# Performance work log

Measured on AMD Instinct MI355X. Metric: run time of the kernel, lower is better.

## Reference

```python
import jax, jax.numpy as jnp
import numpy as np
from jax import lax

DT = 0.1  # forward() default dt


def setup_inputs() -> dict:
    key = jax.random.key(0)
    k1, k2, k3 = jax.random.split(key, 3)
    B, S = 256, 65536
    strain = jax.random.normal(k1, (B, S), dtype=jnp.float32)
    strain_rate = jax.random.normal(k2, (B, S), dtype=jnp.float32)
    log_E = jnp.zeros((1,), dtype=jnp.float32)            # E = 1.0
    log_eta = jnp.log(jnp.full((1,), 10.0, jnp.float32))  # eta = 10.0
    return {"strain": strain, "strain_rate": strain_rate,
            "log_E": log_E, "log_eta": log_eta}


def reference(strain, strain_rate, log_E, log_eta):
    # Maxwell element: stress[0] = E*strain[0] + eta*rate[0]
    #                  stress[t] = a*stress[t-1] + E*(strain[t]-strain[t-1]),  a = exp(-dt/tau)
    E = jnp.exp(log_E)          # (1,)
    eta = jnp.exp(log_eta)      # (1,)
    tau = eta / E
    a = jnp.exp(-DT / tau)      # (1,) constant decay

    B, S = strain.shape
    # driving term u[t]
    u0 = E * strain[:, :1] + eta * strain_rate[:, :1]          # (B,1)
    u_rest = E * (strain[:, 1:] - strain[:, :-1])              # (B,S-1)
    u = jnp.concatenate([u0, u_rest], axis=1)                  # (B,S)
    # decay coeffs: first step has no history
    A = jnp.concatenate([jnp.ones((B, 1), strain.dtype),
                         jnp.broadcast_to(a, (B, S - 1))], axis=1)

    def combine(x, y):
        a1, b1 = x
        a2, b2 = y
        return a1 * a2, b2 + a2 * b1

    _, stress = lax.associative_scan(combine, (A, u), axis=1)  # (B,S)
    return stress
```

## Files before the change

### kernel.cpp

```cpp
#include <hip/hip_runtime.h>
#include <math.h>


#define DT_F     0.1f
#define S_LEN    65536
#define B_ROWS   256
#define CHUNK    8192
#define WARM     2048
#define CPR      (S_LEN / CHUNK)

__global__ __launch_bounds__(256) void maxwell_scan(
    const float* __restrict__ strain,
    const float* __restrict__ rate,
    const float* __restrict__ log_E,
    const float* __restrict__ log_eta,
    float* __restrict__ out)
{
    const int lane = threadIdx.x & 63;
    const int wid  = blockIdx.x * 4 + (threadIdx.x >> 6);
    const int row  = wid / CPR;
    const int c    = wid % CPR;

    const float E   = __expf(log_E[0]);
    const float eta = __expf(log_eta[0]);
    const float lam = -DT_F * E / eta;
    const float a   = __expf(lam);
    const float a2 = a * a, a3 = a2 * a, a4 = a2 * a2;
    const float a8 = a4 * a4, a16 = a8 * a8, a32 = a16 * a16;
    const float a64 = a32 * a32, a128 = a64 * a64, a256 = a128 * a128;
    const float alane = __expf(lam * (float)(4 * lane));

    const int rowbase = row * S_LEN;
    const int t0   = c * CHUNK;
    const int tw   = (c == 0) ? 0 : (t0 - WARM);
    const int tend = t0 + CHUNK;

    const float4* s4 = (const float4*)(strain + rowbase);
    float4*       o4 = (float4*)(out + rowbase);

    float G = 0.0f;
    float last_strain = (tw > 0) ? strain[rowbase + tw - 1] : 0.0f;
    const float u_first = E * strain[rowbase] + eta * rate[rowbase];

    for (int t = tw; t < tend; t += 256) {
        float4 f = s4[(t >> 2) + lane];

        float pf   = __shfl_up(f.w, 1);
        float prev = (lane == 0) ? last_strain : pf;
        float u0 = E * (f.x - prev);
        if (t == 0 && lane == 0) u0 = u_first;
        float u1 = E * (f.y - f.x);
        float u2 = E * (f.z - f.y);
        float u3 = E * (f.w - f.z);

        float s0 = u0;
        float s1 = fmaf(a, s0, u1);
        float s2 = fmaf(a, s1, u2);
        float s3 = fmaf(a, s2, u3);

        float D = s3, v;
        v = __shfl_up(D, 1);  D += (lane >= 1)  ? a4   * v : 0.0f;
        v = __shfl_up(D, 2);  D += (lane >= 2)  ? a8   * v : 0.0f;
        v = __shfl_up(D, 4);  D += (lane >= 4)  ? a16  * v : 0.0f;
        v = __shfl_up(D, 8);  D += (lane >= 8)  ? a32  * v : 0.0f;
        v = __shfl_up(D, 16); D += (lane >= 16) ? a64  * v : 0.0f;
        v = __shfl_up(D, 32); D += (lane >= 32) ? a128 * v : 0.0f;

        float Dm1 = __shfl_up(D, 1);
        float C = (lane == 0) ? 0.0f : Dm1;
        C = fmaf(alane, G, C);

        float o0 = fmaf(a,  C, s0);
        float o1 = fmaf(a2, C, s1);
        float o2 = fmaf(a3, C, s2);
        float o3 = fmaf(a4, C, s3);

        if (t >= t0) {
            o4[(t >> 2) + lane] = make_float4(o0, o1, o2, o3);
        }

        G = fmaf(a256, G, __shfl(D, 63));
        last_strain = __shfl(f.w, 63);
    }
}

extern "C" void kernel_launch(void* const* d_in, const int* in_sizes, int n_in,
                              void* d_out, int out_size, void* d_ws, size_t ws_size,
                              hipStream_t stream) {
    const float* strain  = (const float*)d_in[0];
    const float* rate    = (const float*)d_in[1];
    const float* log_E   = (const float*)d_in[2];
    const float* log_eta = (const float*)d_in[3];
    float* out = (float*)d_out;

    const int total_chunks = B_ROWS * CPR;
    const int blocks = total_chunks / 4;
    maxwell_scan<<<blocks, 256, 0, stream>>>(strain, rate, log_E, log_eta, out);
}
```

Baseline: 176.8 us.

## Process eight elements per lane, shrink chunks, use nontemporal stores

Each lane now handles eight consecutive elements (two float4 loads) per iteration instead of four, so each wave iteration covers 512 elements and the wave-level shuffle scan is amortised over twice the work. The chunk size drops from 8192 to 2048 with a 1024-element warm-up, which raises the number of waves and the parallelism available across the GPU. Output is written with nontemporal stores to avoid polluting the cache. The trade-off is more redundant warm-up reads relative to useful output (half a chunk instead of a quarter), and a shorter warm-up that relies on the decay factor making truncation error negligible.

```diff
diff --git a/kernel.cpp b/kernel.cpp
--- a/kernel.cpp
+++ b/kernel.cpp
@@ -5,9 +5,11 @@
 #define DT_F     0.1f
 #define S_LEN    65536
 #define B_ROWS   256
-#define CHUNK    8192
-#define WARM     2048
+#define CHUNK    2048
+#define WARM     1024
 #define CPR      (S_LEN / CHUNK)
+
+typedef float nfloat4 __attribute__((ext_vector_type(4)));
 
 __global__ __launch_bounds__(256) void maxwell_scan(
     const float* __restrict__ strain,
@@ -25,62 +27,73 @@
     const float eta = __expf(log_eta[0]);
     const float lam = -DT_F * E / eta;
     const float a   = __expf(lam);
-    const float a2 = a * a, a3 = a2 * a, a4 = a2 * a2;
-    const float a8 = a4 * a4, a16 = a8 * a8, a32 = a16 * a16;
-    const float a64 = a32 * a32, a128 = a64 * a64, a256 = a128 * a128;
-    const float alane = __expf(lam * (float)(4 * lane));
+    const float a2 = a * a,     a3 = a2 * a,    a4 = a2 * a2;
+    const float a5 = a4 * a,    a6 = a4 * a2,   a7 = a4 * a3,   a8 = a4 * a4;
+    const float a16 = a8 * a8,  a32 = a16 * a16, a64 = a32 * a32;
+    const float a128 = a64 * a64, a256 = a128 * a128, a512 = a256 * a256;
+    const float alane = __expf(lam * (float)(8 * lane));
 
     const int rowbase = row * S_LEN;
     const int t0   = c * CHUNK;
     const int tw   = (c == 0) ? 0 : (t0 - WARM);
     const int tend = t0 + CHUNK;
 
-    const float4* s4 = (const float4*)(strain + rowbase);
-    float4*       o4 = (float4*)(out + rowbase);
+    const nfloat4* s4 = (const nfloat4*)(strain + rowbase);
+    nfloat4*       o4 = (nfloat4*)(out + rowbase);
 
     float G = 0.0f;
     float last_strain = (tw > 0) ? strain[rowbase + tw - 1] : 0.0f;
     const float u_first = E * strain[rowbase] + eta * rate[rowbase];
 
-    for (int t = tw; t < tend; t += 256) {
-        float4 f = s4[(t >> 2) + lane];
+    for (int t = tw; t < tend; t += 512) {
+        const int vi = (t >> 2) + 2 * lane;
+        nfloat4 f0 = s4[vi];
+        nfloat4 f1 = s4[vi + 1];
 
-        float pf   = __shfl_up(f.w, 1);
+        float pf   = __shfl_up(f1.w, 1);
         float prev = (lane == 0) ? last_strain : pf;
-        float u0 = E * (f.x - prev);
+        float u0 = E * (f0.x - prev);
         if (t == 0 && lane == 0) u0 = u_first;
-        float u1 = E * (f.y - f.x);
-        float u2 = E * (f.z - f.y);
-        float u3 = E * (f.w - f.z);
+        float u1 = E * (f0.y - f0.x);
+        float u2 = E * (f0.z - f0.y);
+        float u3 = E * (f0.w - f0.z);
+        float u4 = E * (f1.x - f0.w);
+        float u5 = E * (f1.y - f1.x);
+        float u6 = E * (f1.z - f1.y);
+        float u7 = E * (f1.w - f1.z);
 
         float s0 = u0;
         float s1 = fmaf(a, s0, u1);
         float s2 = fmaf(a, s1, u2);
         float s3 = fmaf(a, s2, u3);
+        float s4v = fmaf(a, s3, u4);
+        float s5 = fmaf(a, s4v, u5);
+        float s6 = fmaf(a, s5, u6);
+        float s7 = fmaf(a, s6, u7);
 
-        float D = s3, v;
-        v = __shfl_up(D, 1);  D += (lane >= 1)  ? a4   * v : 0.0f;
-        v = __shfl_up(D, 2);  D += (lane >= 2)  ? a8   * v : 0.0f;
-        v = __shfl_up(D, 4);  D += (lane >= 4)  ? a16  * v : 0.0f;
-        v = __shfl_up(D, 8);  D += (lane >= 8)  ? a32  * v : 0.0f;
-        v = __shfl_up(D, 16); D += (lane >= 16) ? a64  * v : 0.0f;
-        v = __shfl_up(D, 32); D += (lane >= 32) ? a128 * v : 0.0f;
+        float D = s7, v;
+        v = __shfl_up(D, 1);  D += (lane >= 1)  ? a8   * v : 0.0f;
+        v = __shfl_up(D, 2);  D += (lane >= 2)  ? a16  * v : 0.0f;
+        v = __shfl_up(D, 4);  D += (lane >= 4)  ? a32  * v : 0.0f;
+        v = __shfl_up(D, 8);  D += (lane >= 8)  ? a64  * v : 0.0f;
+        v = __shfl_up(D, 16); D += (lane >= 16) ? a128 * v : 0.0f;
+        v = __shfl_up(D, 32); D += (lane >= 32) ? a256 * v : 0.0f;
 
         float Dm1 = __shfl_up(D, 1);
         float C = (lane == 0) ? 0.0f : Dm1;
         C = fmaf(alane, G, C);
 
-        float o0 = fmaf(a,  C, s0);
-        float o1 = fmaf(a2, C, s1);
-        float o2 = fmaf(a3, C, s2);
-        float o3 = fmaf(a4, C, s3);
-
         if (t >= t0) {
-            o4[(t >> 2) + lane] = make_float4(o0, o1, o2, o3);
+            nfloat4 o0 = { fmaf(a,  C, s0),  fmaf(a2, C, s1),
+                           fmaf(a3, C, s2),  fmaf(a4, C, s3) };
+            nfloat4 o1 = { fmaf(a5, C, s4v), fmaf(a6, C, s5),
+                           fmaf(a7, C, s6),  fmaf(a8, C, s7) };
+            __builtin_nontemporal_store(o0, &o4[vi]);
+            __builtin_nontemporal_store(o1, &o4[vi + 1]);
         }
 
-        G = fmaf(a256, G, __shfl(D, 63));
-        last_strain = __shfl(f.w, 63);
+        G = fmaf(a512, G, __shfl(D, 63));
+        last_strain = __shfl(f1.w, 63);
     }
 }
 
```

Result: faster. 164.5 us (-6.9%).

## Reformulate Maxwell scan on raw strain with DPP row scans and smaller chunks

Applied to the files above, without the earlier changes.

Rewrites the recurrence algebraically to scan the strain values directly (stress = E*strain + E(a-1)*scan of previous strain, plus a decaying rate term), which removes the neighbour-difference shuffle. The intra-wave scan uses DPP row shifts within 16-lane rows plus readlane to combine rows, replacing six cross-lane shuffles with conditional masks. Chunks shrink to 2048 with a 1024-element warm-up and all payload loads are issued up front, fully unrolled, for more parallelism and memory-level overlap. This trades a higher warm-up overhead ratio and different floating-point rounding for cheaper per-step lane communication.

```diff
diff --git a/kernel.cpp b/kernel.cpp
--- a/kernel.cpp
+++ b/kernel.cpp
@@ -2,12 +2,23 @@
 #include <math.h>
 
 
-#define DT_F     0.1f
-#define S_LEN    65536
-#define B_ROWS   256
-#define CHUNK    8192
-#define WARM     2048
-#define CPR      (S_LEN / CHUNK)
+#define DT_F  0.1f
+#define S_LEN 65536
+#define B_ROWS 256
+#define CHUNK 2048
+#define WARM  1024
+#define CPR   (S_LEN / CHUNK)
+
+typedef float nfloat4 __attribute__((ext_vector_type(4)));
+
+template<int N>
+__device__ __forceinline__ float dpp_shr(float x) {
+    return __int_as_float(__builtin_amdgcn_update_dpp(
+        0, __float_as_int(x), 0x110 + N, 0xF, 0xF, false));
+}
+__device__ __forceinline__ float rdl(float x, int l) {
+    return __int_as_float(__builtin_amdgcn_readlane(__float_as_int(x), l));
+}
 
 __global__ __launch_bounds__(256) void maxwell_scan(
     const float* __restrict__ strain,
@@ -25,63 +36,90 @@
     const float eta = __expf(log_eta[0]);
     const float lam = -DT_F * E / eta;
     const float a   = __expf(lam);
-    const float a2 = a * a, a3 = a2 * a, a4 = a2 * a2;
-    const float a8 = a4 * a4, a16 = a8 * a8, a32 = a16 * a16;
-    const float a64 = a32 * a32, a128 = a64 * a64, a256 = a128 * a128;
+    const float a2 = a * a, a3 = a2 * a, a4 = a2 * a2, a8 = a4 * a4;
+    const float a16 = a8 * a8, a32 = a16 * a16, a64 = a32 * a32;
+    const float a128 = a64 * a64, a256 = a128 * a128;
+    const float cc = E * (a - 1.0f);
+    const float cca1 = cc * a, cca2 = cc * a2, cca3 = cc * a3;
+
+    const int  lrow = lane & 15;
     const float alane = __expf(lam * (float)(4 * lane));
+    const float wX    = __expf(lam * (float)(4 * lrow));
+    const bool row0 = (lrow == 0);
+    const bool ge16 = lane >= 16, ge32 = lane >= 32, ge48 = lane >= 48;
 
     const int rowbase = row * S_LEN;
-    const int t0   = c * CHUNK;
-    const int tw   = (c == 0) ? 0 : (t0 - WARM);
-    const int tend = t0 + CHUNK;
+    const int t0 = c * CHUNK;
+    const nfloat4* s4 = (const nfloat4*)(strain + rowbase);
+    nfloat4*       o4 = (nfloat4*)(out + rowbase);
 
-    const float4* s4 = (const float4*)(strain + rowbase);
-    float4*       o4 = (float4*)(out + rowbase);
+    const int vp = (t0 >> 2) + lane;
+    nfloat4 p0 = s4[vp +   0], p1 = s4[vp +  64], p2 = s4[vp + 128], p3 = s4[vp + 192];
+    nfloat4 p4 = s4[vp + 256], p5 = s4[vp + 320], p6 = s4[vp + 384], p7 = s4[vp + 448];
 
-    float G = 0.0f;
-    float last_strain = (tw > 0) ? strain[rowbase + tw - 1] : 0.0f;
-    const float u_first = E * strain[rowbase] + eta * rate[rowbase];
+    float S = 0.0f;
 
-    for (int t = tw; t < tend; t += 256) {
-        float4 f = s4[(t >> 2) + lane];
+    if (c != 0) {
+        const int vw = ((t0 - WARM) >> 2) + lane;
+        nfloat4 w0 = s4[vw], w1 = s4[vw + 64], w2 = s4[vw + 128], w3 = s4[vw + 192];
+        auto warmg = [&](nfloat4 wf) {
+            float fl = wf.x;
+            fl = fmaf(a, fl, wf.y); fl = fmaf(a, fl, wf.z); fl = fmaf(a, fl, wf.w);
+            float D = fl, v;
+            v = dpp_shr<1>(D); D = fmaf(a4,  v, D);
+            v = dpp_shr<2>(D); D = fmaf(a8,  v, D);
+            v = dpp_shr<4>(D); D = fmaf(a16, v, D);
+            v = dpp_shr<8>(D); D = fmaf(a32, v, D);
+            float r15 = rdl(D, 15), r31 = rdl(D, 31), r47 = rdl(D, 47), r63 = rdl(D, 63);
+            float P1 = r15;
+            float P2 = fmaf(a64, P1, r31);
+            float P3 = fmaf(a64, P2, r47);
+            float T  = fmaf(a64, P3, r63);
+            S = fmaf(a256, S, T);
+        };
+        warmg(w0); warmg(w1); warmg(w2); warmg(w3);
+    }
 
-        float pf   = __shfl_up(f.w, 1);
-        float prev = (lane == 0) ? last_strain : pf;
-        float u0 = E * (f.x - prev);
-        if (t == 0 && lane == 0) u0 = u_first;
-        float u1 = E * (f.y - f.x);
-        float u2 = E * (f.z - f.y);
-        float u3 = E * (f.w - f.z);
+    float etar0 = 0.0f;
+    if (c == 0) etar0 = eta * rate[rowbase];
+    const float rl0 = etar0 * alane;
+    const float rl1 = rl0 * a, rl2 = rl0 * a2, rl3 = rl0 * a3;
+    float base = 1.0f;
 
-        float s0 = u0;
-        float s1 = fmaf(a, s0, u1);
-        float s2 = fmaf(a, s1, u2);
-        float s3 = fmaf(a, s2, u3);
-
-        float D = s3, v;
-        v = __shfl_up(D, 1);  D += (lane >= 1)  ? a4   * v : 0.0f;
-        v = __shfl_up(D, 2);  D += (lane >= 2)  ? a8   * v : 0.0f;
-        v = __shfl_up(D, 4);  D += (lane >= 4)  ? a16  * v : 0.0f;
-        v = __shfl_up(D, 8);  D += (lane >= 8)  ? a32  * v : 0.0f;
-        v = __shfl_up(D, 16); D += (lane >= 16) ? a64  * v : 0.0f;
-        v = __shfl_up(D, 32); D += (lane >= 32) ? a128 * v : 0.0f;
-
-        float Dm1 = __shfl_up(D, 1);
-        float C = (lane == 0) ? 0.0f : Dm1;
-        C = fmaf(alane, G, C);
-
-        float o0 = fmaf(a,  C, s0);
-        float o1 = fmaf(a2, C, s1);
-        float o2 = fmaf(a3, C, s2);
-        float o3 = fmaf(a4, C, s3);
-
-        if (t >= t0) {
-            o4[(t >> 2) + lane] = make_float4(o0, o1, o2, o3);
-        }
-
-        G = fmaf(a256, G, __shfl(D, 63));
-        last_strain = __shfl(f.w, 63);
-    }
+    auto payg = [&](nfloat4 pf, int gi) {
+        float fl0 = pf.x;
+        float fl1 = fmaf(a, fl0, pf.y);
+        float fl2 = fmaf(a, fl1, pf.z);
+        float fl3 = fmaf(a, fl2, pf.w);
+        float D = fl3, v;
+        v = dpp_shr<1>(D); D = fmaf(a4,  v, D);
+        v = dpp_shr<2>(D); D = fmaf(a8,  v, D);
+        v = dpp_shr<4>(D); D = fmaf(a16, v, D);
+        v = dpp_shr<8>(D); D = fmaf(a32, v, D);
+        float r15 = rdl(D, 15), r31 = rdl(D, 31), r47 = rdl(D, 47), r63 = rdl(D, 63);
+        float P1 = r15;
+        float P2 = fmaf(a64, P1, r31);
+        float P3 = fmaf(a64, P2, r47);
+        float T  = fmaf(a64, P3, r63);
+        float Pv = ge48 ? P3 : (ge32 ? P2 : (ge16 ? P1 : 0.0f));
+        float Xd = dpp_shr<1>(D);
+        float X  = row0 ? Pv : fmaf(wX, Pv, Xd);
+        float Xs = fmaf(alane, S, X);
+        nfloat4 o;
+        o.x = fmaf(cc,   Xs, E * pf.x);
+        o.y = fmaf(cca1, Xs, fmaf(cc, fl0, E * pf.y));
+        o.z = fmaf(cca2, Xs, fmaf(cc, fl1, E * pf.z));
+        o.w = fmaf(cca3, Xs, fmaf(cc, fl2, E * pf.w));
+        o.x = fmaf(base, rl0, o.x);
+        o.y = fmaf(base, rl1, o.y);
+        o.z = fmaf(base, rl2, o.z);
+        o.w = fmaf(base, rl3, o.w);
+        o4[vp + gi * 64] = o;
+        S = fmaf(a256, S, T);
+        base *= a256;
+    };
+    payg(p0, 0); payg(p1, 1); payg(p2, 2); payg(p3, 3);
+    payg(p4, 4); payg(p5, 5); payg(p6, 6); payg(p7, 7);
 }
 
 extern "C" void kernel_launch(void* const* d_in, const int* in_sizes, int n_in,
```

Measured after the change: 158.9 us. 1.11x faster.
